# Optimization experiments

Measured on AMD Instinct MI355X. Metric: run time of the kernel, lower is better.

## Reference

```python
import jax, jax.numpy as jnp
import numpy as np

N_NODES = 100000


def _gcn_norm(edge_index, num_nodes):
    # PyG GCNConv default: add self-loops, symmetric normalization.
    src, dst = edge_index[0], edge_index[1]
    loop = jnp.arange(num_nodes, dtype=src.dtype)
    src = jnp.concatenate([src, loop])
    dst = jnp.concatenate([dst, loop])
    deg = jax.ops.segment_sum(jnp.ones_like(dst, dtype=jnp.float32), dst,
                              num_segments=num_nodes)
    dinv = jnp.where(deg > 0, jax.lax.rsqrt(jnp.maximum(deg, 1.0)), 0.0)
    norm = dinv[src] * dinv[dst]  # [E + N]
    return src, dst, norm


def _gcn_layer(x, src, dst, norm, W, b, num_nodes):
    h = x @ W                              # [N, out]
    msg = h[src] * norm[:, None]           # gather + scale, [E+N, out]
    agg = jax.ops.segment_sum(msg, dst, num_segments=num_nodes)  # scatter-add
    return agg + b


def setup_inputs() -> dict:
    key = jax.random.key(0)
    ks = jax.random.split(key, 12)
    in_c, hid = 64, 128
    dims = [in_c, hid, hid // 2, hid // 4, hid // 8, 1]
    x = jax.random.normal(ks[0], (N_NODES, in_c), dtype=jnp.float32)
    edge_index = jax.random.randint(ks[1], (2, 1600000), 0, N_NODES,
                                    dtype=jnp.int64)
    inp = {"x": x, "edge_index": edge_index}
    for i in range(5):
        fan_in = dims[i]
        s = 1.0 / np.sqrt(fan_in)
        inp[f"W{i+1}"] = jax.random.uniform(ks[2 + 2 * i], (dims[i], dims[i + 1]),
                                            minval=-s, maxval=s,
                                            dtype=jnp.float32)
        inp[f"b{i+1}"] = jnp.zeros((dims[i + 1],), dtype=jnp.float32)
    return inp


def reference(x, edge_index, W1, b1, W2, b2, W3, b3, W4, b4, W5, b5):
    num_nodes = x.shape[0]
    src, dst, norm = _gcn_norm(edge_index, num_nodes)
    h = _gcn_layer(x, src, dst, norm, W1, b1, num_nodes)
    h = jax.nn.relu(h)
    h = _gcn_layer(h, src, dst, norm, W2, b2, num_nodes)
    h = jax.nn.relu(h)
    h = _gcn_layer(h, src, dst, norm, W3, b3, num_nodes)
    h = jax.nn.relu(h)
    h = _gcn_layer(h, src, dst, norm, W4, b4, num_nodes)
    h = jax.nn.relu(h)
    h = _gcn_layer(h, src, dst, norm, W5, b5, num_nodes)
    return h
```

## Files before the change

kernel.cpp:

```cpp
#include <hip/hip_runtime.h>
#include <math.h>


#define NBIN_MAX 256
#define BSHIFT 9
#define BINW 512
#define CHUNK 8192

__global__ __launch_bounds__(256) void k_hist(const int* __restrict__ dst, int E,
                                              int nbin, int* __restrict__ binCnt) {
    __shared__ int h[NBIN_MAX];
    int t = threadIdx.x;
    for (int i = t; i < nbin; i += 256) h[i] = 0;
    __syncthreads();
    for (int e = blockIdx.x * 256 + t; e < E; e += gridDim.x * 256)
        atomicAdd(&h[dst[e] >> BSHIFT], 1);
    __syncthreads();
    for (int i = t; i < nbin; i += 256)
        if (h[i]) atomicAdd(&binCnt[i], h[i]);
}

__global__ __launch_bounds__(256) void k_binscan(const int* __restrict__ binCnt,
                                                 int nbin, int* __restrict__ binBase,
                                                 int* __restrict__ binCur) {
    __shared__ int sh[256];
    int t = threadIdx.x;
    int v = (t < nbin) ? binCnt[t] : 0;
    sh[t] = v;
    __syncthreads();
    for (int d = 1; d < 256; d <<= 1) {
        int u = (t >= d) ? sh[t - d] : 0;
        __syncthreads();
        sh[t] += u;
        __syncthreads();
    }
    int ex = sh[t] - v;
    if (t < nbin) { binBase[t] = ex; binCur[t] = ex; }
    if (t == nbin - 1) binBase[nbin] = sh[t];
}

__global__ __launch_bounds__(256) void k_binfill(const int* __restrict__ src,
                                                 const int* __restrict__ dst, int E,
                                                 int nbin, int* __restrict__ binCur,
                                                 unsigned* __restrict__ tmp) {
    __shared__ int h[NBIN_MAX];
    __shared__ int res[NBIN_MAX];
    int t = threadIdx.x;
    int e0 = blockIdx.x * CHUNK;
    int e1 = min(e0 + CHUNK, E);
    for (int i = t; i < nbin; i += 256) h[i] = 0;
    __syncthreads();
    for (int e = e0 + t; e < e1; e += 256)
        atomicAdd(&h[dst[e] >> BSHIFT], 1);
    __syncthreads();
    for (int i = t; i < nbin; i += 256)
        res[i] = h[i] ? atomicAdd(&binCur[i], h[i]) : 0;
    __syncthreads();
    for (int i = t; i < nbin; i += 256) h[i] = 0;
    __syncthreads();
    for (int e = e0 + t; e < e1; e += 256) {
        int d = dst[e];
        int b = d >> BSHIFT;
        int p = res[b] + atomicAdd(&h[b], 1);
        tmp[p] = ((unsigned)src[e] << BSHIFT) | (unsigned)(d & (BINW - 1));
    }
}

__global__ __launch_bounds__(256) void k_csr(const unsigned* __restrict__ tmp,
                                             const int* __restrict__ binBase,
                                             int n, int nbin,
                                             float* __restrict__ dinv,
                                             int* __restrict__ offs,
                                             int* __restrict__ csr) {
    __shared__ int ldeg[BINW];
    __shared__ int loff[BINW];
    __shared__ int pair[256];
    int b = blockIdx.x;
    int t = threadIdx.x;
    ldeg[t] = 0; ldeg[t + 256] = 0;
    __syncthreads();
    int lo = binBase[b], hi = binBase[b + 1];
    for (int p = lo + t; p < hi; p += 256)
        atomicAdd(&ldeg[tmp[p] & (BINW - 1u)], 1);
    __syncthreads();
    int a0 = ldeg[2 * t], a1 = ldeg[2 * t + 1];
    pair[t] = a0 + a1;
    __syncthreads();
    int v = pair[t];
    for (int d = 1; d < 256; d <<= 1) {
        int u = (t >= d) ? pair[t - d] : 0;
        __syncthreads();
        pair[t] += u;
        __syncthreads();
    }
    int ex = pair[t] - v;
    loff[2 * t] = ex;
    loff[2 * t + 1] = ex + a0;
    __syncthreads();
    int v0 = b << BSHIFT;
    for (int i = t; i < BINW; i += 256) {
        int vv = v0 + i;
        if (vv < n) {
            offs[vv] = lo + loff[i];
            dinv[vv] = 1.0f / sqrtf((float)(ldeg[i] + 1));
        }
    }
    if (t == 0 && b == nbin - 1) offs[n] = hi;
    __syncthreads();
    ldeg[t] = 0; ldeg[t + 256] = 0;
    __syncthreads();
    for (int p = lo + t; p < hi; p += 256) {
        unsigned u = tmp[p];
        int d0 = (int)(u & (BINW - 1u));
        int pos = loff[d0] + atomicAdd(&ldeg[d0], 1);
        csr[lo + pos] = (int)(u >> BSHIFT);
    }
}

__global__ __launch_bounds__(256) void k_agg_l1(const float* __restrict__ X,
                                                const float* __restrict__ dinv,
                                                const int* __restrict__ offs,
                                                const int* __restrict__ csr,
                                                float* __restrict__ Y, int n) {
    constexpr int W = 64;
    int t = blockIdx.x * 256 + threadIdx.x;
    int v = t / W, c = t % W;
    if (v >= n) return;
    float dv = dinv[v];
    float sum = X[(size_t)v * W + c] * dv;
    int e = offs[v], re = offs[v + 1];
    for (; e + 4 <= re; e += 4) {
        int u0 = csr[e], u1 = csr[e + 1], u2 = csr[e + 2], u3 = csr[e + 3];
        float a0 = X[(size_t)u0 * W + c] * dinv[u0];
        float a1 = X[(size_t)u1 * W + c] * dinv[u1];
        float a2 = X[(size_t)u2 * W + c] * dinv[u2];
        float a3 = X[(size_t)u3 * W + c] * dinv[u3];
        sum += a0 + a1 + a2 + a3;
    }
    for (; e < re; ++e) { int u = csr[e]; sum += X[(size_t)u * W + c] * dinv[u]; }
    Y[(size_t)v * W + c] = dv * sum;
}

template <int W, bool RELU>
__global__ __launch_bounds__(256) void k_agg(const float* __restrict__ S,
                                             const float* __restrict__ dinv,
                                             const int* __restrict__ offs,
                                             const int* __restrict__ csr,
                                             const float* __restrict__ bg,
                                             float* __restrict__ Y, int n) {
    int t = blockIdx.x * 256 + threadIdx.x;
    int v = t / W, c = t % W;
    if (v >= n) return;
    float sum = S[(size_t)v * W + c];
    int e = offs[v], re = offs[v + 1];
    for (; e + 4 <= re; e += 4) {
        int u0 = csr[e], u1 = csr[e + 1], u2 = csr[e + 2], u3 = csr[e + 3];
        float a0 = S[(size_t)u0 * W + c];
        float a1 = S[(size_t)u1 * W + c];
        float a2 = S[(size_t)u2 * W + c];
        float a3 = S[(size_t)u3 * W + c];
        sum += a0 + a1 + a2 + a3;
    }
    for (; e < re; ++e) sum += S[(size_t)csr[e] * W + c];
    float r = dinv[v] * sum + bg[c];
    if (RELU) r = fmaxf(r, 0.0f);
    Y[(size_t)v * W + c] = r;
}

template <int IN, int OUT, int EPI>
__global__ __launch_bounds__(256) void k_gemm(const float* __restrict__ X,
                                              const float* __restrict__ Wg,
                                              const float* __restrict__ bg,
                                              const float* __restrict__ dinv,
                                              float* __restrict__ Y, int nrows) {
    constexpr int TPR = OUT / 4;
    constexpr int GROUPS = 256 / TPR;
    constexpr int ROWS = GROUPS * 2;
    __shared__ __align__(16) float Wl[IN * OUT];
    __shared__ __align__(16) float xl[ROWS * IN];
    __shared__ float bl[OUT];
    int tid = threadIdx.x;
    for (int i = tid; i < IN * OUT; i += 256) Wl[i] = Wg[i];
    if (EPI == 0)
        for (int i = tid; i < OUT; i += 256) bl[i] = bg[i];
    int base = blockIdx.x * ROWS;
    for (int i = tid; i < ROWS * IN; i += 256) {
        int r = base + i / IN;
        xl[i] = (r < nrows) ? X[(size_t)base * IN + i] : 0.0f;
    }
    __syncthreads();
    int g = tid / TPR;
    int c0 = (tid % TPR) * 4;
    int r0 = base + g * 2, r1 = r0 + 1;
    int l0 = (g * 2) * IN, l1 = l0 + IN;
    float4 acc0 = make_float4(0.f, 0.f, 0.f, 0.f);
    float4 acc1 = make_float4(0.f, 0.f, 0.f, 0.f);
#pragma unroll 8
    for (int k = 0; k < IN; ++k) {
        float4 w = *(const float4*)&Wl[k * OUT + c0];
        float a0 = xl[l0 + k], a1 = xl[l1 + k];
        acc0.x += a0 * w.x; acc0.y += a0 * w.y; acc0.z += a0 * w.z; acc0.w += a0 * w.w;
        acc1.x += a1 * w.x; acc1.y += a1 * w.y; acc1.z += a1 * w.z; acc1.w += a1 * w.w;
    }
    if (EPI == 0) {
        float bx = bl[c0], by = bl[c0 + 1], bz = bl[c0 + 2], bw = bl[c0 + 3];
        acc0.x = fmaxf(acc0.x + bx, 0.f); acc0.y = fmaxf(acc0.y + by, 0.f);
        acc0.z = fmaxf(acc0.z + bz, 0.f); acc0.w = fmaxf(acc0.w + bw, 0.f);
        acc1.x = fmaxf(acc1.x + bx, 0.f); acc1.y = fmaxf(acc1.y + by, 0.f);
        acc1.z = fmaxf(acc1.z + bz, 0.f); acc1.w = fmaxf(acc1.w + bw, 0.f);
    } else {
        if (r0 < nrows) { float d0 = dinv[r0]; acc0.x *= d0; acc0.y *= d0; acc0.z *= d0; acc0.w *= d0; }
        if (r1 < nrows) { float d1 = dinv[r1]; acc1.x *= d1; acc1.y *= d1; acc1.z *= d1; acc1.w *= d1; }
    }
    if (r0 < nrows) *(float4*)&Y[(size_t)r0 * OUT + c0] = acc0;
    if (r1 < nrows) *(float4*)&Y[(size_t)r1 * OUT + c0] = acc1;
}

__global__ __launch_bounds__(256) void k_gemm5(const float* __restrict__ X,
                                               const float* __restrict__ Wg,
                                               const float* __restrict__ dinv,
                                               float* __restrict__ Y, int n) {
    int r = blockIdx.x * 256 + threadIdx.x;
    if (r >= n) return;
    float acc = 0.f;
#pragma unroll
    for (int k = 0; k < 16; ++k) acc += X[(size_t)r * 16 + k] * Wg[k];
    Y[r] = acc * dinv[r];
}

extern "C" void kernel_launch(void* const* d_in, const int* in_sizes, int n_in,
                              void* d_out, int out_size, void* d_ws, size_t ws_size,
                              hipStream_t stream) {
    const float* x  = (const float*)d_in[0];
    const int*   ei = (const int*)d_in[1];
    const float* W1 = (const float*)d_in[2];  const float* b1 = (const float*)d_in[3];
    const float* W2 = (const float*)d_in[4];  const float* b2 = (const float*)d_in[5];
    const float* W3 = (const float*)d_in[6];  const float* b3 = (const float*)d_in[7];
    const float* W4 = (const float*)d_in[8];  const float* b4 = (const float*)d_in[9];
    const float* W5 = (const float*)d_in[10]; const float* b5 = (const float*)d_in[11];

    const int N = in_sizes[0] / 64;
    const int E = in_sizes[1] / 2;
    const int* src = ei;
    const int* dst = ei + E;
    const int nbin = (N + BINW - 1) / BINW;

    char* ws = (char*)d_ws;
    size_t off = 0;
    auto alloc = [&](size_t bytes) -> void* {
        void* p = ws + off;
        off = (off + bytes + 255) & ~(size_t)255;
        return p;
    };
    float* dinv    = (float*)alloc((size_t)N * 4);
    int*   offs    = (int*)alloc((size_t)(N + 1) * 4);
    int*   binCnt  = (int*)alloc((size_t)NBIN_MAX * 4);
    int*   binBase = (int*)alloc((size_t)(NBIN_MAX + 1) * 4);
    int*   binCur  = (int*)alloc((size_t)NBIN_MAX * 4);
    int*   csr     = (int*)alloc((size_t)E * 4);
    float* A       = (float*)alloc((size_t)N * 128 * 4);
    float* B       = (float*)alloc((size_t)N * 64 * 4);
    float* C       = (float*)alloc((size_t)N * 64 * 4);
    unsigned* tmp  = (unsigned*)C;

    hipMemsetAsync(binCnt, 0, (size_t)NBIN_MAX * 4, stream);

    k_hist<<<256, 256, 0, stream>>>(dst, E, nbin, binCnt);
    k_binscan<<<1, 256, 0, stream>>>(binCnt, nbin, binBase, binCur);
    k_binfill<<<(E + CHUNK - 1) / CHUNK, 256, 0, stream>>>(src, dst, E, nbin, binCur, tmp);
    k_csr<<<nbin, 256, 0, stream>>>(tmp, binBase, N, nbin, dinv, offs, csr);

    k_agg_l1<<<(N * 64 + 255) / 256, 256, 0, stream>>>(x, dinv, offs, csr, B, N);
    k_gemm<64, 128, 0><<<(N + 15) / 16, 256, 0, stream>>>(B, W1, b1, nullptr, A, N);
    k_gemm<128, 64, 1><<<(N + 31) / 32, 256, 0, stream>>>(A, W2, nullptr, dinv, B, N);
    k_agg<64, true><<<(N * 64 + 255) / 256, 256, 0, stream>>>(B, dinv, offs, csr, b2, C, N);
    k_gemm<64, 32, 1><<<(N + 63) / 64, 256, 0, stream>>>(C, W3, nullptr, dinv, B, N);
    k_agg<32, true><<<(N * 32 + 255) / 256, 256, 0, stream>>>(B, dinv, offs, csr, b3, A, N);
    k_gemm<32, 16, 1><<<(N + 127) / 128, 256, 0, stream>>>(A, W4, nullptr, dinv, B, N);
    k_agg<16, true><<<(N * 16 + 255) / 256, 256, 0, stream>>>(B, dinv, offs, csr, b4, C, N);
    k_gemm5<<<(N + 255) / 256, 256, 0, stream>>>(C, W5, dinv, B, N);
    k_agg<1, false><<<(N + 255) / 256, 256, 0, stream>>>(B, dinv, offs, csr, b5, (float*)d_out, N);
}
```

Before: 417.3 us.

## Use wave-per-node float4 aggregation and fuse last aggregation with final GEMV

Replaces the thread-per-feature CSR aggregation with a wave-per-node scheme. Lanes are split into groups that each handle different neighbours, load float4 feature slices, and combine their partial sums with xor shuffles. The width-16 aggregation is fused with the layer-5 matrix-vector product, which drops one kernel and one intermediate write/read. This should raise memory-level parallelism and vectorise the gathers, at the cost of shuffle reductions and idle lanes for low-degree nodes.

```diff
diff --git a/kernel.cpp b/kernel.cpp
--- a/kernel.cpp
+++ b/kernel.cpp
@@ -117,54 +117,132 @@
     }
 }
 
-__global__ __launch_bounds__(256) void k_agg_l1(const float* __restrict__ X,
-                                                const float* __restrict__ dinv,
-                                                const int* __restrict__ offs,
-                                                const int* __restrict__ csr,
-                                                float* __restrict__ Y, int n) {
-    constexpr int W = 64;
-    int t = blockIdx.x * 256 + threadIdx.x;
-    int v = t / W, c = t % W;
+template <int W, bool RELU, bool BIAS, bool L1SCALE>
+__global__ __launch_bounds__(256) void k_aggv(const float* __restrict__ S,
+                                              const float* __restrict__ dinv,
+                                              const int* __restrict__ offs,
+                                              const int* __restrict__ csr,
+                                              const float* __restrict__ bg,
+                                              float* __restrict__ Y, int n) {
+    constexpr int LPR = W / 4;
+    constexpr int G = 64 / LPR;
+    int lane = threadIdx.x & 63;
+    int wave = threadIdx.x >> 6;
+    int v = blockIdx.x * 4 + wave;
     if (v >= n) return;
+    int g = lane / LPR;
+    int j = lane % LPR;
     float dv = dinv[v];
-    float sum = X[(size_t)v * W + c] * dv;
+    float4 acc0 = make_float4(0.f, 0.f, 0.f, 0.f);
+    float4 acc1 = make_float4(0.f, 0.f, 0.f, 0.f);
+    if (g == 0) {
+        float4 xv = *(const float4*)&S[(size_t)v * W + j * 4];
+        float sc = L1SCALE ? dv : 1.0f;
+        acc0.x = xv.x * sc; acc0.y = xv.y * sc; acc0.z = xv.z * sc; acc0.w = xv.w * sc;
+    }
+    int e0 = offs[v], re = offs[v + 1];
+    for (int eb = e0; eb < re; eb += 2 * G) {
+        int ea = eb + g, ec = eb + G + g;
+        if (ea < re) {
+            int u = csr[ea];
+            float4 a = *(const float4*)&S[(size_t)u * W + j * 4];
+            float sc = L1SCALE ? dinv[u] : 1.0f;
+            acc0.x += a.x * sc; acc0.y += a.y * sc; acc0.z += a.z * sc; acc0.w += a.w * sc;
+        }
+        if (ec < re) {
+            int u = csr[ec];
+            float4 a = *(const float4*)&S[(size_t)u * W + j * 4];
+            float sc = L1SCALE ? dinv[u] : 1.0f;
+            acc1.x += a.x * sc; acc1.y += a.y * sc; acc1.z += a.z * sc; acc1.w += a.w * sc;
+        }
+    }
+    acc0.x += acc1.x; acc0.y += acc1.y; acc0.z += acc1.z; acc0.w += acc1.w;
+#pragma unroll
+    for (int d = LPR; d < 64; d <<= 1) {
+        acc0.x += __shfl_xor(acc0.x, d);
+        acc0.y += __shfl_xor(acc0.y, d);
+        acc0.z += __shfl_xor(acc0.z, d);
+        acc0.w += __shfl_xor(acc0.w, d);
+    }
+    if (lane < LPR) {
+        float4 r;
+        r.x = dv * acc0.x; r.y = dv * acc0.y; r.z = dv * acc0.z; r.w = dv * acc0.w;
+        if (BIAS) {
+            float4 bv = *(const float4*)&bg[j * 4];
+            r.x += bv.x; r.y += bv.y; r.z += bv.z; r.w += bv.w;
+        }
+        if (RELU) {
+            r.x = fmaxf(r.x, 0.f); r.y = fmaxf(r.y, 0.f);
+            r.z = fmaxf(r.z, 0.f); r.w = fmaxf(r.w, 0.f);
+        }
+        *(float4*)&Y[(size_t)v * W + j * 4] = r;
+    }
+}
+
+__global__ __launch_bounds__(256) void k_agg16_gemm5(const float* __restrict__ S,
+                                                     const float* __restrict__ dinv,
+                                                     const int* __restrict__ offs,
+                                                     const int* __restrict__ csr,
+                                                     const float* __restrict__ b4,
+                                                     const float* __restrict__ W5,
+                                                     float* __restrict__ Y, int n) {
+    constexpr int W = 16, LPR = 4, G = 16;
+    int lane = threadIdx.x & 63;
+    int wave = threadIdx.x >> 6;
+    int v = blockIdx.x * 4 + wave;
+    if (v >= n) return;
+    int g = lane / LPR;
+    int j = lane % LPR;
+    float dv = dinv[v];
+    float4 acc0 = make_float4(0.f, 0.f, 0.f, 0.f);
+    float4 acc1 = make_float4(0.f, 0.f, 0.f, 0.f);
+    if (g == 0) acc0 = *(const float4*)&S[(size_t)v * W + j * 4];
+    int e0 = offs[v], re = offs[v + 1];
+    for (int eb = e0; eb < re; eb += 2 * G) {
+        int ea = eb + g, ec = eb + G + g;
+        if (ea < re) {
+            int u = csr[ea];
+            float4 a = *(const float4*)&S[(size_t)u * W + j * 4];
+            acc0.x += a.x; acc0.y += a.y; acc0.z += a.z; acc0.w += a.w;
+        }
+        if (ec < re) {
+            int u = csr[ec];
+            float4 a = *(const float4*)&S[(size_t)u * W + j * 4];
+            acc1.x += a.x; acc1.y += a.y; acc1.z += a.z; acc1.w += a.w;
+        }
+    }
+    acc0.x += acc1.x; acc0.y += acc1.y; acc0.z += acc1.z; acc0.w += acc1.w;
+#pragma unroll
+    for (int d = LPR; d < 64; d <<= 1) {
+        acc0.x += __shfl_xor(acc0.x, d);
+        acc0.y += __shfl_xor(acc0.y, d);
+        acc0.z += __shfl_xor(acc0.z, d);
+        acc0.w += __shfl_xor(acc0.w, d);
+    }
+    float4 bv = *(const float4*)&b4[j * 4];
+    float4 w5 = *(const float4*)&W5[j * 4];
+    float hx = fmaxf(dv * acc0.x + bv.x, 0.f);
+    float hy = fmaxf(dv * acc0.y + bv.y, 0.f);
+    float hz = fmaxf(dv * acc0.z + bv.z, 0.f);
+    float hw = fmaxf(dv * acc0.w + bv.w, 0.f);
+    float p = hx * w5.x + hy * w5.y + hz * w5.z + hw * w5.w;
+    p += __shfl_xor(p, 1);
+    p += __shfl_xor(p, 2);
+    if (lane == 0) Y[v] = p * dv;
+}
+
+__global__ __launch_bounds__(256) void k_agg1(const float* __restrict__ S,
+                                              const float* __restrict__ dinv,
+                                              const int* __restrict__ offs,
+                                              const int* __restrict__ csr,
+                                              const float* __restrict__ bg,
+                                              float* __restrict__ Y, int n) {
+    int v = blockIdx.x * 256 + threadIdx.x;
+    if (v >= n) return;
+    float sum = S[v];
     int e = offs[v], re = offs[v + 1];
-    for (; e + 4 <= re; e += 4) {
-        int u0 = csr[e], u1 = csr[e + 1], u2 = csr[e + 2], u3 = csr[e + 3];
-        float a0 = X[(size_t)u0 * W + c] * dinv[u0];
-        float a1 = X[(size_t)u1 * W + c] * dinv[u1];
-        float a2 = X[(size_t)u2 * W + c] * dinv[u2];
-        float a3 = X[(size_t)u3 * W + c] * dinv[u3];
-        sum += a0 + a1 + a2 + a3;
-    }
-    for (; e < re; ++e) { int u = csr[e]; sum += X[(size_t)u * W + c] * dinv[u]; }
-    Y[(size_t)v * W + c] = dv * sum;
-}
-
-template <int W, bool RELU>
-__global__ __launch_bounds__(256) void k_agg(const float* __restrict__ S,
-                                             const float* __restrict__ dinv,
-                                             const int* __restrict__ offs,
-                                             const int* __restrict__ csr,
-                                             const float* __restrict__ bg,
-                                             float* __restrict__ Y, int n) {
-    int t = blockIdx.x * 256 + threadIdx.x;
-    int v = t / W, c = t % W;
-    if (v >= n) return;
-    float sum = S[(size_t)v * W + c];
-    int e = offs[v], re = offs[v + 1];
-    for (; e + 4 <= re; e += 4) {
-        int u0 = csr[e], u1 = csr[e + 1], u2 = csr[e + 2], u3 = csr[e + 3];
-        float a0 = S[(size_t)u0 * W + c];
-        float a1 = S[(size_t)u1 * W + c];
-        float a2 = S[(size_t)u2 * W + c];
-        float a3 = S[(size_t)u3 * W + c];
-        sum += a0 + a1 + a2 + a3;
-    }
-    for (; e < re; ++e) sum += S[(size_t)csr[e] * W + c];
-    float r = dinv[v] * sum + bg[c];
-    if (RELU) r = fmaxf(r, 0.0f);
-    Y[(size_t)v * W + c] = r;
+    for (; e < re; ++e) sum += S[csr[e]];
+    Y[v] = dinv[v] * sum + bg[0];
 }
 
 template <int IN, int OUT, int EPI>
@@ -216,18 +294,6 @@
     if (r1 < nrows) *(float4*)&Y[(size_t)r1 * OUT + c0] = acc1;
 }
 
-__global__ __launch_bounds__(256) void k_gemm5(const float* __restrict__ X,
-                                               const float* __restrict__ Wg,
-                                               const float* __restrict__ dinv,
-                                               float* __restrict__ Y, int n) {
-    int r = blockIdx.x * 256 + threadIdx.x;
-    if (r >= n) return;
-    float acc = 0.f;
-#pragma unroll
-    for (int k = 0; k < 16; ++k) acc += X[(size_t)r * 16 + k] * Wg[k];
-    Y[r] = acc * dinv[r];
-}
-
 extern "C" void kernel_launch(void* const* d_in, const int* in_sizes, int n_in,
                               void* d_out, int out_size, void* d_ws, size_t ws_size,
                               hipStream_t stream) {
@@ -258,6 +324,7 @@
     int*   binBase = (int*)alloc((size_t)(NBIN_MAX + 1) * 4);
     int*   binCur  = (int*)alloc((size_t)NBIN_MAX * 4);
     int*   csr     = (int*)alloc((size_t)E * 4);
+    float* s5      = (float*)alloc((size_t)N * 4);
     float* A       = (float*)alloc((size_t)N * 128 * 4);
     float* B       = (float*)alloc((size_t)N * 64 * 4);
     float* C       = (float*)alloc((size_t)N * 64 * 4);
@@ -270,14 +337,14 @@
     k_binfill<<<(E + CHUNK - 1) / CHUNK, 256, 0, stream>>>(src, dst, E, nbin, binCur, tmp);
     k_csr<<<nbin, 256, 0, stream>>>(tmp, binBase, N, nbin, dinv, offs, csr);
 
-    k_agg_l1<<<(N * 64 + 255) / 256, 256, 0, stream>>>(x, dinv, offs, csr, B, N);
+    const int gagg = (N + 3) / 4;
+    k_aggv<64, false, false, true><<<gagg, 256, 0, stream>>>(x, dinv, offs, csr, nullptr, B, N);
     k_gemm<64, 128, 0><<<(N + 15) / 16, 256, 0, stream>>>(B, W1, b1, nullptr, A, N);
     k_gemm<128, 64, 1><<<(N + 31) / 32, 256, 0, stream>>>(A, W2, nullptr, dinv, B, N);
-    k_agg<64, true><<<(N * 64 + 255) / 256, 256, 0, stream>>>(B, dinv, offs, csr, b2, C, N);
+    k_aggv<64, true, true, false><<<gagg, 256, 0, stream>>>(B, dinv, offs, csr, b2, C, N);
     k_gemm<64, 32, 1><<<(N + 63) / 64, 256, 0, stream>>>(C, W3, nullptr, dinv, B, N);
-    k_agg<32, true><<<(N * 32 + 255) / 256, 256, 0, stream>>>(B, dinv, offs, csr, b3, A, N);
+    k_aggv<32, true, true, false><<<gagg, 256, 0, stream>>>(B, dinv, offs, csr, b3, A, N);
     k_gemm<32, 16, 1><<<(N + 127) / 128, 256, 0, stream>>>(A, W4, nullptr, dinv, B, N);
-    k_agg<16, true><<<(N * 16 + 255) / 256, 256, 0, stream>>>(B, dinv, offs, csr, b4, C, N);
-    k_gemm5<<<(N + 255) / 256, 256, 0, stream>>>(C, W5, dinv, B, N);
-    k_agg<1, false><<<(N + 255) / 256, 256, 0, stream>>>(B, dinv, offs, csr, b5, (float*)d_out, N);
-}
+    k_agg16_gemm5<<<gagg, 256, 0, stream>>>(B, dinv, offs, csr, b4, W5, s5, N);
+    k_agg1<<<(N + 255) / 256, 256, 0, stream>>>(s5, dinv, offs, csr, b5, (float*)d_out, N);
+}
```

Measured after the change: 424.8 us. Within noise of the previous version (+1.8%).
